# Optimization experiments

Measured on AMD Instinct MI355X. Metric: run time of the kernel, lower is better.

The kernel has to match this reference:

```python
import jax, jax.numpy as jnp
import numpy as np
import math

B, N, D = 16, 1024, 1024

def setup_inputs() -> dict:
    key = jax.random.key(0)
    k1, k2, k3, k4 = jax.random.split(key, 4)
    x = jax.random.normal(k1, (B, N, D), dtype=jnp.float32)
    # Keras 'random_normal' initializer defaults to stddev=0.05
    w_keys = jax.random.normal(k2, (N, N), dtype=jnp.float32) * 0.05
    w_queries = jax.random.normal(k3, (N, N), dtype=jnp.float32) * 0.05
    w_values = jax.random.normal(k4, (N, N), dtype=jnp.float32) * 0.05
    return {"x": x, "w_keys": w_keys, "w_queries": w_queries, "w_values": w_values}

def reference(x, w_keys, w_queries, w_values):
    # x: (B, N, D); weights: (N, N); fact = sqrt(N) per build(input_shape[1])
    fact = math.sqrt(x.shape[1])
    ip = jnp.swapaxes(x, 1, 2)              # (B, D, N)
    vk = ip @ w_keys                         # (B, D, N)
    vq = ip @ w_queries                      # (B, D, N)
    vv = ip @ w_values                       # (B, D, N)
    kq = jnp.einsum('bdn,ben->bde', vk, vq) / fact   # (B, D, D)
    sm = jax.nn.softmax(kq, axis=-1)         # softmax over last axis
    # tf: sm @ transpose(pm(vv)) == sm @ vv  since pm then transpose_b cancel
    out = jnp.einsum('bde,ben->bdn', sm, vv) # (B, D, N)
    return jnp.swapaxes(out, 1, 2)           # (B, N, D)
```

## Files before the change

### kernel.cpp

```cpp
#include <hip/hip_runtime.h>
#include <stdint.h>


typedef __bf16 bf16x8_t __attribute__((ext_vector_type(8)));
typedef float  f32x4_t  __attribute__((ext_vector_type(4)));

typedef __attribute__((address_space(3))) uint32_t as3_u32;
typedef __attribute__((address_space(1))) uint32_t as1_u32;

__device__ __forceinline__ void async_copy16(const void* g, const void* l) {
  __builtin_amdgcn_global_load_lds((const as1_u32*)(uintptr_t)g,
                                   (as3_u32*)(uint32_t)(uintptr_t)l,
                                   16, 0, 0);
}

__device__ __forceinline__ uint16_t f2bf(float f) {
  uint32_t x = __float_as_uint(f);
  return (uint16_t)((x + 0x7fffu + ((x >> 16) & 1u)) >> 16);
}
__device__ __forceinline__ float bf2f(uint16_t b) {
  return __uint_as_float(((uint32_t)b) << 16);
}

template <bool OUT_F32>
__global__ __launch_bounds__(256, 4)
void gemm_bt(const uint16_t* __restrict__ A, const uint16_t* __restrict__ B,
             void* __restrict__ Cv, int K, int ldc,
             size_t sA, size_t sB, size_t sC, float alpha)
{
  __shared__ __align__(16) char smem[32768];
  char* As = smem;
  char* Bs = smem + 16384;

  const int lid  = blockIdx.x;
  const int xcd  = lid & 7;
  const int slot = lid >> 3;
  const int z    = (xcd << 1) | (slot >> 6);
  const int t64  = slot & 63;
  const int bm0  = (t64 >> 3) << 7;
  const int bn0  = (t64 & 7) << 7;

  A += (size_t)z * sA;
  B += (size_t)z * sB;

  const int t    = threadIdx.x;
  const int lane = t & 63;
  const int w    = t >> 6;
  const int q    = lane >> 4;
  const int r16  = lane & 15;
  const int wm   = (w >> 1) << 6;
  const int wn   = (w & 1) << 6;

  f32x4_t acc[4][4];
#pragma unroll
  for (int i = 0; i < 4; i++)
#pragma unroll
    for (int j = 0; j < 4; j++) acc[i][j] = (f32x4_t){0.f, 0.f, 0.f, 0.f};

  for (int k0 = 0; k0 < K; k0 += 64) {
#pragma unroll
    for (int i = 0; i < 4; i++) {
      const int o  = (i << 12) + (t << 4);
      const int m  = o >> 7;
      const int cp = (o >> 4) & 7;
      const int c  = cp ^ (m & 7);
      async_copy16(A + (size_t)(bm0 + m) * K + (size_t)(k0 + (c << 3)), As + o);
      async_copy16(B + (size_t)(bn0 + m) * K + (size_t)(k0 + (c << 3)), Bs + o);
    }
    __syncthreads();

#pragma unroll
    for (int kk = 0; kk < 2; kk++) {
      bf16x8_t af[4], bfr[4];
#pragma unroll
      for (int mi = 0; mi < 4; mi++) {
        const int m = wm + (mi << 4) + r16;
        const int c = (kk << 2) + q;
        af[mi] = *(const bf16x8_t*)(As + (m << 7) + ((c ^ (m & 7)) << 4));
      }
#pragma unroll
      for (int ni = 0; ni < 4; ni++) {
        const int n = wn + (ni << 4) + r16;
        const int c = (kk << 2) + q;
        bfr[ni] = *(const bf16x8_t*)(Bs + (n << 7) + ((c ^ (n & 7)) << 4));
      }
#pragma unroll
      for (int mi = 0; mi < 4; mi++)
#pragma unroll
        for (int ni = 0; ni < 4; ni++)
          acc[mi][ni] = __builtin_amdgcn_mfma_f32_16x16x32_bf16(
              af[mi], bfr[ni], acc[mi][ni], 0, 0, 0);
    }
    __syncthreads();
  }

  if (OUT_F32) {
    float* C = (float*)Cv + (size_t)z * sC;
#pragma unroll
    for (int mi = 0; mi < 4; mi++)
#pragma unroll
      for (int ni = 0; ni < 4; ni++)
#pragma unroll
        for (int r = 0; r < 4; r++) {
          const int row = bm0 + wm + (mi << 4) + (q << 2) + r;
          const int col = bn0 + wn + (ni << 4) + r16;
          C[(size_t)row * ldc + col] = acc[mi][ni][r] * alpha;
        }
  } else {
    float* reg = (float*)smem + (size_t)w * (16 * 66);
    uint16_t* C = (uint16_t*)Cv + (size_t)z * sC;
#pragma unroll
    for (int mi = 0; mi < 4; mi++) {
#pragma unroll
      for (int ni = 0; ni < 4; ni++)
#pragma unroll
        for (int r = 0; r < 4; r++)
          reg[((q << 2) + r) * 66 + (ni << 4) + r16] = acc[mi][ni][r] * alpha;
#pragma unroll
      for (int it = 0; it < 8; it++) {
        const int rr = (it << 1) + (lane >> 5);
        const int cc = (lane & 31) << 1;
        const float2 v = *(const float2*)(reg + rr * 66 + cc);
        const uint32_t p = (uint32_t)f2bf(v.x) | ((uint32_t)f2bf(v.y) << 16);
        const int row = bm0 + wm + (mi << 4) + rr;
        const int col = bn0 + wn + cc;
        *(uint32_t*)(C + (size_t)row * ldc + col) = p;
      }
    }
  }
}

__global__ __launch_bounds__(256)
void transpose_cast(const float* __restrict__ src, uint16_t* __restrict__ dst,
                    int R, int Ccols, size_t sStride, size_t dStride)
{
  __shared__ float tile[32][33];
  const int z = blockIdx.z;
  src += (size_t)z * sStride;
  dst += (size_t)z * dStride;
  const int c0 = blockIdx.x << 5;
  const int r0 = blockIdx.y << 5;
  const int tx = threadIdx.x;
  const int ty = threadIdx.y;
#pragma unroll
  for (int i = 0; i < 32; i += 8)
    tile[ty + i][tx] = src[(size_t)(r0 + ty + i) * Ccols + (c0 + tx)];
  __syncthreads();
#pragma unroll
  for (int i = 0; i < 32; i += 8)
    dst[(size_t)(c0 + ty + i) * R + (r0 + tx)] = f2bf(tile[tx][ty + i]);
}

__global__ __launch_bounds__(256)
void transpose_cast_w(const float* __restrict__ w0, const float* __restrict__ w1,
                      const float* __restrict__ w2, uint16_t* __restrict__ o0,
                      uint16_t* __restrict__ o1, uint16_t* __restrict__ o2)
{
  __shared__ float tile[32][33];
  const int z = blockIdx.z;
  const float* src = (z == 0) ? w0 : (z == 1) ? w1 : w2;
  uint16_t* dst = (z == 0) ? o0 : (z == 1) ? o1 : o2;
  const int c0 = blockIdx.x << 5;
  const int r0 = blockIdx.y << 5;
  const int tx = threadIdx.x;
  const int ty = threadIdx.y;
#pragma unroll
  for (int i = 0; i < 32; i += 8)
    tile[ty + i][tx] = src[(size_t)(r0 + ty + i) * 1024 + (c0 + tx)];
  __syncthreads();
#pragma unroll
  for (int i = 0; i < 32; i += 8)
    dst[(size_t)(c0 + ty + i) * 1024 + (r0 + tx)] = f2bf(tile[tx][ty + i]);
}

__global__ __launch_bounds__(256)
void softmax_rows(const uint16_t* __restrict__ in, uint16_t* __restrict__ out)
{
  const size_t row = blockIdx.x;
  const ushort4* p4 = (const ushort4*)(in + row * 1024);
  ushort4* o4 = (ushort4*)(out + row * 1024);
  const int t = threadIdx.x;
  const int lane = t & 63;
  const int wv = t >> 6;

  const ushort4 u = p4[t];
  float v0 = bf2f(u.x), v1 = bf2f(u.y), v2 = bf2f(u.z), v3 = bf2f(u.w);

  float m = fmaxf(fmaxf(v0, v1), fmaxf(v2, v3));
#pragma unroll
  for (int s = 32; s; s >>= 1) m = fmaxf(m, __shfl_xor(m, s, 64));
  __shared__ float red[8];
  if (lane == 0) red[wv] = m;
  __syncthreads();
  m = fmaxf(fmaxf(red[0], red[1]), fmaxf(red[2], red[3]));

  const float e0 = __expf(v0 - m), e1 = __expf(v1 - m);
  const float e2 = __expf(v2 - m), e3 = __expf(v3 - m);
  float s = e0 + e1 + e2 + e3;
#pragma unroll
  for (int sh = 32; sh; sh >>= 1) s += __shfl_xor(s, sh, 64);
  if (lane == 0) red[4 + wv] = s;
  __syncthreads();
  s = red[4] + red[5] + red[6] + red[7];

  const float inv = 1.0f / s;
  ushort4 r;
  r.x = f2bf(e0 * inv); r.y = f2bf(e1 * inv);
  r.z = f2bf(e2 * inv); r.w = f2bf(e3 * inv);
  o4[t] = r;
}

extern "C" void kernel_launch(void* const* d_in, const int* in_sizes, int n_in,
                              void* d_out, int out_size, void* d_ws, size_t ws_size,
                              hipStream_t stream)
{
  const float* x  = (const float*)d_in[0];
  const float* wk = (const float*)d_in[1];
  const float* wq = (const float*)d_in[2];
  const float* wv = (const float*)d_in[3];
  float* out = (float*)d_out;

  constexpr int BB = 16, N = 1024, D = 1024;
  constexpr size_t DN = (size_t)D * N;

  char* ws = (char*)d_ws;
  uint16_t* xT  = (uint16_t*)(ws);
  uint16_t* Wtk = (uint16_t*)(ws + (32ull << 20));
  uint16_t* Wtq = (uint16_t*)(ws + (34ull << 20));
  uint16_t* Wtv = (uint16_t*)(ws + (36ull << 20));
  uint16_t* vk  = (uint16_t*)(ws + (38ull << 20));
  uint16_t* vq  = (uint16_t*)(ws + (70ull << 20));
  uint16_t* vvT = (uint16_t*)(ws + (102ull << 20));
  uint16_t* kq  = xT;
  uint16_t* sm  = vk;

  const dim3 tb(32, 8);
  transpose_cast<<<dim3(D / 32, N / 32, BB), tb, 0, stream>>>(x, xT, N, D, DN, DN);
  transpose_cast_w<<<dim3(N / 32, N / 32, 3), tb, 0, stream>>>(wk, wq, wv,
                                                               Wtk, Wtq, Wtv);

  gemm_bt<false><<<1024, 256, 0, stream>>>(xT, Wtk, vk, 1024, 1024, DN, 0, DN, 1.0f);
  gemm_bt<false><<<1024, 256, 0, stream>>>(xT, Wtq, vq, 1024, 1024, DN, 0, DN, 1.0f);
  gemm_bt<false><<<1024, 256, 0, stream>>>(Wtv, xT, vvT, 1024, 1024, 0, DN, DN, 1.0f);
  gemm_bt<false><<<1024, 256, 0, stream>>>(vk, vq, kq, 1024, 1024, DN, DN, DN, 0.03125f);
  softmax_rows<<<BB * D, 256, 0, stream>>>(kq, sm);
  gemm_bt<true><<<1024, 256, 0, stream>>>(vvT, sm, out, 1024, 1024, DN, DN, DN, 1.0f);
}
```

Baseline: 333.3 us.

## Replace GEMM with 256x256-tile double-buffered pipelined kernel using 512 threads

Replaces the 128x128 single-buffered GEMM with a 256x256 tile kernel of 8 waves. It double-buffers 128KB of LDS and interleaves async global-to-LDS loads of the next K slice with MFMA quadrants of the current one, using explicit waitcnt, barriers and setprio. The larger tile raises data reuse per loaded byte, and the prefetch hides load latency. In exchange, the grid shrinks to 256 blocks (one per CU), so occupancy is lower and there are no spare waves to cover stalls. The hand-ordered barriers and waitcnts are fragile.

After: 316.6 us. 5.0% less time.

```diff
diff --git a/kernel.cpp b/kernel.cpp
--- a/kernel.cpp
+++ b/kernel.cpp
@@ -23,108 +23,203 @@
 }
 
 template <bool OUT_F32>
-__global__ __launch_bounds__(256, 4)
-void gemm_bt(const uint16_t* __restrict__ A, const uint16_t* __restrict__ B,
-             void* __restrict__ Cv, int K, int ldc,
-             size_t sA, size_t sB, size_t sC, float alpha)
-{
-  __shared__ __align__(16) char smem[32768];
-  char* As = smem;
-  char* Bs = smem + 16384;
+__global__ __launch_bounds__(512, 2)
+void gemm_bt256(const uint16_t* __restrict__ A, const uint16_t* __restrict__ B,
+                void* __restrict__ Cv, size_t sA, size_t sB, size_t sC,
+                float alpha)
+{
+  __shared__ __align__(16) char smem[131072];
 
   const int lid  = blockIdx.x;
   const int xcd  = lid & 7;
   const int slot = lid >> 3;
-  const int z    = (xcd << 1) | (slot >> 6);
-  const int t64  = slot & 63;
-  const int bm0  = (t64 >> 3) << 7;
-  const int bn0  = (t64 & 7) << 7;
-
-  A += (size_t)z * sA;
-  B += (size_t)z * sB;
+  const int z    = (xcd << 1) | (slot >> 4);
+  const int t16  = slot & 15;
+  const int bm0  = (t16 >> 2) << 8;
+  const int bn0  = (t16 & 3) << 8;
+
+  A += (size_t)z * sA + ((size_t)bm0 << 10);
+  B += (size_t)z * sB + ((size_t)bn0 << 10);
 
   const int t    = threadIdx.x;
   const int lane = t & 63;
   const int w    = t >> 6;
   const int q    = lane >> 4;
   const int r16  = lane & 15;
-  const int wm   = (w >> 1) << 6;
-  const int wn   = (w & 1) << 6;
-
-  f32x4_t acc[4][4];
-#pragma unroll
-  for (int i = 0; i < 4; i++)
+  const int wm   = (w >> 2) << 7;
+  const int wn   = (w & 3) << 6;
+
+  const int g0  = t >> 3;
+  const int cp  = t & 7;
+  const int ce  = (cp ^ (g0 & 7)) << 3;
+  const int sAo = (g0 << 7) + (cp << 4);
+  const int rB  = ((g0 >> 5) << 6) + (g0 & 31);
+  const int sBo = (rB << 7) + (cp << 4);
+  const uint16_t* Ab = A + ((size_t)g0 << 10) + ce;
+  const uint16_t* Bb = B + ((size_t)rB << 10) + ce;
+
+#define STAGE_A(s, kge, dst) do {                                              \
+    async_copy16(Ab + (((s)*64 +   0) << 10) + (kge),                          \
+                 smem + (dst) + sAo + (s)*8192);                               \
+    async_copy16(Ab + (((s)*64 + 128) << 10) + (kge),                          \
+                 smem + (dst) + sAo + (s)*8192 + 16384);                       \
+  } while (0)
+#define STAGE_B(s, kge, dst) do {                                              \
+    async_copy16(Bb + (((s)*32 +   0) << 10) + (kge),                          \
+                 smem + (dst) + 32768 + sBo + (s)*4096);                       \
+    async_copy16(Bb + (((s)*32 + 128) << 10) + (kge),                          \
+                 smem + (dst) + 32768 + sBo + (s)*4096 + 16384);               \
+  } while (0)
+
+  const int sl0 = ((0 + q) ^ (r16 & 7)) << 4;
+  const int sl1 = ((4 + q) ^ (r16 & 7)) << 4;
+  int aRd0 = ((wm + r16) << 7) + sl0;
+  int aRd1 = ((wm + r16) << 7) + sl1;
+  int bRd0 = 32768 + ((wn + r16) << 7) + sl0;
+  int bRd1 = 32768 + ((wn + r16) << 7) + sl1;
+
+  f32x4_t acc[8][4];
+#pragma unroll
+  for (int i = 0; i < 8; i++)
 #pragma unroll
     for (int j = 0; j < 4; j++) acc[i][j] = (f32x4_t){0.f, 0.f, 0.f, 0.f};
 
-  for (int k0 = 0; k0 < K; k0 += 64) {
-#pragma unroll
-    for (int i = 0; i < 4; i++) {
-      const int o  = (i << 12) + (t << 4);
-      const int m  = o >> 7;
-      const int cp = (o >> 4) & 7;
-      const int c  = cp ^ (m & 7);
-      async_copy16(A + (size_t)(bm0 + m) * K + (size_t)(k0 + (c << 3)), As + o);
-      async_copy16(B + (size_t)(bn0 + m) * K + (size_t)(k0 + (c << 3)), Bs + o);
-    }
-    __syncthreads();
-
-#pragma unroll
-    for (int kk = 0; kk < 2; kk++) {
-      bf16x8_t af[4], bfr[4];
-#pragma unroll
-      for (int mi = 0; mi < 4; mi++) {
-        const int m = wm + (mi << 4) + r16;
-        const int c = (kk << 2) + q;
-        af[mi] = *(const bf16x8_t*)(As + (m << 7) + ((c ^ (m & 7)) << 4));
-      }
-#pragma unroll
-      for (int ni = 0; ni < 4; ni++) {
-        const int n = wn + (ni << 4) + r16;
-        const int c = (kk << 2) + q;
-        bfr[ni] = *(const bf16x8_t*)(Bs + (n << 7) + ((c ^ (n & 7)) << 4));
-      }
-#pragma unroll
-      for (int mi = 0; mi < 4; mi++)
-#pragma unroll
-        for (int ni = 0; ni < 4; ni++)
+  STAGE_A(0, 0, 0);
+  STAGE_B(0, 0, 0);
+  STAGE_B(1, 0, 0);
+  STAGE_A(1, 0, 0);
+  asm volatile("s_waitcnt vmcnt(4)" ::: "memory");
+  __builtin_amdgcn_s_barrier();
+
+  int nxt = 65536;
+  for (int t0 = 0; t0 < 16; ++t0) {
+    const int kge = ((t0 + 1) & 15) << 6;
+    bf16x8_t af[4][2], bfA[2][2], bfB[2][2];
+
+#pragma unroll
+    for (int mi = 0; mi < 4; ++mi) {
+      af[mi][0] = *(const bf16x8_t*)(smem + aRd0 + mi * 2048);
+      af[mi][1] = *(const bf16x8_t*)(smem + aRd1 + mi * 2048);
+    }
+#pragma unroll
+    for (int ni = 0; ni < 2; ++ni) {
+      bfA[ni][0] = *(const bf16x8_t*)(smem + bRd0 + ni * 2048);
+      bfA[ni][1] = *(const bf16x8_t*)(smem + bRd1 + ni * 2048);
+    }
+    STAGE_A(0, kge, nxt);
+    asm volatile("s_waitcnt vmcnt(4)" ::: "memory");
+    __builtin_amdgcn_s_barrier();
+    asm volatile("s_waitcnt lgkmcnt(0)" ::: "memory");
+    __builtin_amdgcn_sched_barrier(0);
+    __builtin_amdgcn_s_setprio(1);
+#pragma unroll
+    for (int kk = 0; kk < 2; ++kk)
+#pragma unroll
+      for (int mi = 0; mi < 4; ++mi)
+#pragma unroll
+        for (int ni = 0; ni < 2; ++ni)
           acc[mi][ni] = __builtin_amdgcn_mfma_f32_16x16x32_bf16(
-              af[mi], bfr[ni], acc[mi][ni], 0, 0, 0);
-    }
-    __syncthreads();
+              af[mi][kk], bfA[ni][kk], acc[mi][ni], 0, 0, 0);
+    __builtin_amdgcn_s_setprio(0);
+    __builtin_amdgcn_s_barrier();
+
+#pragma unroll
+    for (int ni = 0; ni < 2; ++ni) {
+      bfB[ni][0] = *(const bf16x8_t*)(smem + bRd0 + 4096 + ni * 2048);
+      bfB[ni][1] = *(const bf16x8_t*)(smem + bRd1 + 4096 + ni * 2048);
+    }
+    STAGE_B(0, kge, nxt);
+    asm volatile("s_waitcnt vmcnt(4)" ::: "memory");
+    __builtin_amdgcn_s_barrier();
+    asm volatile("s_waitcnt lgkmcnt(0)" ::: "memory");
+    __builtin_amdgcn_sched_barrier(0);
+    __builtin_amdgcn_s_setprio(1);
+#pragma unroll
+    for (int kk = 0; kk < 2; ++kk)
+#pragma unroll
+      for (int mi = 0; mi < 4; ++mi)
+#pragma unroll
+        for (int ni = 0; ni < 2; ++ni)
+          acc[mi][2 + ni] = __builtin_amdgcn_mfma_f32_16x16x32_bf16(
+              af[mi][kk], bfB[ni][kk], acc[mi][2 + ni], 0, 0, 0);
+    __builtin_amdgcn_s_setprio(0);
+    __builtin_amdgcn_s_barrier();
+
+#pragma unroll
+    for (int mi = 0; mi < 4; ++mi) {
+      af[mi][0] = *(const bf16x8_t*)(smem + aRd0 + 8192 + mi * 2048);
+      af[mi][1] = *(const bf16x8_t*)(smem + aRd1 + 8192 + mi * 2048);
+    }
+    STAGE_B(1, kge, nxt);
+    __builtin_amdgcn_s_barrier();
+    asm volatile("s_waitcnt lgkmcnt(0)" ::: "memory");
+    __builtin_amdgcn_sched_barrier(0);
+    __builtin_amdgcn_s_setprio(1);
+#pragma unroll
+    for (int kk = 0; kk < 2; ++kk)
+#pragma unroll
+      for (int mi = 0; mi < 4; ++mi)
+#pragma unroll
+        for (int ni = 0; ni < 2; ++ni)
+          acc[4 + mi][2 + ni] = __builtin_amdgcn_mfma_f32_16x16x32_bf16(
+              af[mi][kk], bfB[ni][kk], acc[4 + mi][2 + ni], 0, 0, 0);
+    __builtin_amdgcn_s_setprio(0);
+    __builtin_amdgcn_s_barrier();
+
+    STAGE_A(1, kge, nxt);
+    asm volatile("s_waitcnt vmcnt(4)" ::: "memory");
+    __builtin_amdgcn_s_barrier();
+    __builtin_amdgcn_s_setprio(1);
+#pragma unroll
+    for (int kk = 0; kk < 2; ++kk)
+#pragma unroll
+      for (int mi = 0; mi < 4; ++mi)
+#pragma unroll
+        for (int ni = 0; ni < 2; ++ni)
+          acc[4 + mi][ni] = __builtin_amdgcn_mfma_f32_16x16x32_bf16(
+              af[mi][kk], bfA[ni][kk], acc[4 + mi][ni], 0, 0, 0);
+    __builtin_amdgcn_s_setprio(0);
+    __builtin_amdgcn_s_barrier();
+
+    aRd0 ^= 65536; aRd1 ^= 65536; bRd0 ^= 65536; bRd1 ^= 65536; nxt ^= 65536;
   }
+#undef STAGE_A
+#undef STAGE_B
+
+  asm volatile("s_waitcnt vmcnt(0)" ::: "memory");
+  __builtin_amdgcn_s_barrier();
 
   if (OUT_F32) {
     float* C = (float*)Cv + (size_t)z * sC;
 #pragma unroll
-    for (int mi = 0; mi < 4; mi++)
-#pragma unroll
-      for (int ni = 0; ni < 4; ni++)
-#pragma unroll
-        for (int r = 0; r < 4; r++) {
+    for (int mi = 0; mi < 8; ++mi)
+#pragma unroll
+      for (int ni = 0; ni < 4; ++ni)
+#pragma unroll
+        for (int r = 0; r < 4; ++r) {
           const int row = bm0 + wm + (mi << 4) + (q << 2) + r;
           const int col = bn0 + wn + (ni << 4) + r16;
-          C[(size_t)row * ldc + col] = acc[mi][ni][r] * alpha;
+          C[((size_t)row << 10) + col] = acc[mi][ni][r] * alpha;
         }
   } else {
-    float* reg = (float*)smem + (size_t)w * (16 * 66);
+    float* reg = (float*)smem + (size_t)w * 1056;
     uint16_t* C = (uint16_t*)Cv + (size_t)z * sC;
 #pragma unroll
-    for (int mi = 0; mi < 4; mi++) {
-#pragma unroll
-      for (int ni = 0; ni < 4; ni++)
-#pragma unroll
-        for (int r = 0; r < 4; r++)
+    for (int mi = 0; mi < 8; ++mi) {
+#pragma unroll
+      for (int ni = 0; ni < 4; ++ni)
+#pragma unroll
+        for (int r = 0; r < 4; ++r)
           reg[((q << 2) + r) * 66 + (ni << 4) + r16] = acc[mi][ni][r] * alpha;
 #pragma unroll
-      for (int it = 0; it < 8; it++) {
+      for (int it = 0; it < 8; ++it) {
         const int rr = (it << 1) + (lane >> 5);
         const int cc = (lane & 31) << 1;
         const float2 v = *(const float2*)(reg + rr * 66 + cc);
         const uint32_t p = (uint32_t)f2bf(v.x) | ((uint32_t)f2bf(v.y) << 16);
         const int row = bm0 + wm + (mi << 4) + rr;
         const int col = bn0 + wn + cc;
-        *(uint32_t*)(C + (size_t)row * ldc + col) = p;
+        *(uint32_t*)(C + ((size_t)row << 10) + col) = p;
       }
     }
   }
@@ -239,10 +334,10 @@
   transpose_cast_w<<<dim3(N / 32, N / 32, 3), tb, 0, stream>>>(wk, wq, wv,
                                                                Wtk, Wtq, Wtv);
 
-  gemm_bt<false><<<1024, 256, 0, stream>>>(xT, Wtk, vk, 1024, 1024, DN, 0, DN, 1.0f);
-  gemm_bt<false><<<1024, 256, 0, stream>>>(xT, Wtq, vq, 1024, 1024, DN, 0, DN, 1.0f);
-  gemm_bt<false><<<1024, 256, 0, stream>>>(Wtv, xT, vvT, 1024, 1024, 0, DN, DN, 1.0f);
-  gemm_bt<false><<<1024, 256, 0, stream>>>(vk, vq, kq, 1024, 1024, DN, DN, DN, 0.03125f);
+  gemm_bt256<false><<<256, 512, 0, stream>>>(xT, Wtk, vk, DN, 0, DN, 1.0f);
+  gemm_bt256<false><<<256, 512, 0, stream>>>(xT, Wtq, vq, DN, 0, DN, 1.0f);
+  gemm_bt256<false><<<256, 512, 0, stream>>>(Wtv, xT, vvT, 0, DN, DN, 1.0f);
+  gemm_bt256<false><<<256, 512, 0, stream>>>(vk, vq, kq, DN, DN, DN, 0.03125f);
   softmax_rows<<<BB * D, 256, 0, stream>>>(kq, sm);
-  gemm_bt<true><<<1024, 256, 0, stream>>>(vvT, sm, out, 1024, 1024, DN, DN, DN, 1.0f);
-}
+  gemm_bt256<true><<<256, 512, 0, stream>>>(vvT, sm, out, DN, DN, DN, 1.0f);
+}
```
